# Kernel optimization log

Hardware: AMD Instinct MI355X
Metric: run time of the kernel (lower is better)

Reference implementation:

```python
import jax, jax.numpy as jnp
import numpy as np

OUT_FEATURES = 11008
IN_FEATURES = 4096
GROUP_SIZE = 32
NUM_GROUPS = OUT_FEATURES * IN_FEATURES // GROUP_SIZE        # 1,409,024
NUM_PACKED = NUM_GROUPS * (GROUP_SIZE // 8 * 3)              # 16,908,288 bytes


def block_dequantize_3bit(weight_q3, weight_norm):
    """Unpack 3-bit codes (8 values per 3 bytes) and dequantize to fp32."""
    p = weight_q3.reshape(-1, 3).astype(jnp.int32)  # [N/8, 3] bytes
    b0, b1, b2 = p[:, 0], p[:, 1], p[:, 2]
    q = jnp.stack([
        b0 & 7,
        (b0 >> 3) & 7,
        ((b0 >> 6) & 3) | ((b1 & 1) << 2),
        (b1 >> 1) & 7,
        (b1 >> 4) & 7,
        ((b1 >> 7) & 1) | ((b2 & 3) << 1),
        (b2 >> 2) & 7,
        (b2 >> 5) & 7,
    ], axis=-1)                                     # [N/8, 8] codes in 0..7
    q = q.reshape(NUM_GROUPS, GROUP_SIZE).astype(jnp.float32)
    norm = weight_norm.astype(jnp.float32)[:, None]  # [num_groups, 1]
    w = (q / 7.0) * 2.0 * norm - norm                # map [0,7] -> [-norm, norm]
    return w.reshape(OUT_FEATURES, IN_FEATURES)


def setup_inputs() -> dict:
    key = jax.random.key(0)
    k1, k2, k3, k4 = jax.random.split(key, 4)
    x = jax.random.normal(k1, (4, 128, IN_FEATURES), dtype=jnp.float32)
    weight_q3 = jax.random.randint(k2, (NUM_PACKED,), 0, 256, dtype=jnp.int32)
    weight_norm = (jax.random.uniform(k3, (NUM_GROUPS,), dtype=jnp.float32) * 0.1 + 0.01).astype(jnp.float16)
    bias = jax.random.normal(k4, (OUT_FEATURES,), dtype=jnp.float32) * 0.02
    return {"x": x, "weight_q3": weight_q3, "weight_norm": weight_norm, "bias": bias}


def reference(x, weight_q3, weight_norm, bias):
    w = block_dequantize_3bit(weight_q3, weight_norm)  # [out, in] fp32
    return jnp.einsum('bsd,od->bso', x, w) + bias
```

## Files before the change

### kernel.cpp

```cpp
#include <hip/hip_runtime.h>
#include <hip/hip_fp16.h>

#define M_TOTAL 512
#define N_TOTAL 11008
#define K_TOTAL 4096
#define BM 256
#define BN 32
#define BK 64
#define NT (K_TOTAL / BK)
#define NUM_GROUPS (N_TOTAL * K_TOTAL / 32)
#define LDK 72

typedef short bf16x8 __attribute__((ext_vector_type(8)));
typedef _Float16 f16x8 __attribute__((ext_vector_type(8)));
typedef _Float16 f16x2 __attribute__((ext_vector_type(2)));
typedef float f32x4 __attribute__((ext_vector_type(4)));

__device__ __forceinline__ unsigned int pack2_bf16(float f0, float f1) {
    unsigned int u0 = __builtin_bit_cast(unsigned int, f0) + 0x8000u;
    unsigned int u1 = __builtin_bit_cast(unsigned int, f1) + 0x8000u;
    return (u0 >> 16) | (u1 & 0xFFFF0000u);
}

__device__ __forceinline__ void async_ld16(void* lds, const void* g) {
    __builtin_amdgcn_global_load_lds(
        (const __attribute__((address_space(1))) unsigned int*)g,
        (__attribute__((address_space(3))) unsigned int*)lds, 16, 0, 0);
}

__device__ __forceinline__ int detect_mode_wave(const void* __restrict__ wn) {
    const int lane = threadIdx.x & 63;
    const unsigned short* u16 = (const unsigned short*)wn;
    const float* f32p = (const float*)wn;
    const float vb = __builtin_bit_cast(float, (unsigned int)u16[lane] << 16);
    const float vh = __half2float(__builtin_bit_cast(__half, u16[lane]));
    const float vf = f32p[lane];
    const unsigned long long mb = __ballot(vb > 0.005f && vb < 0.12f);
    const unsigned long long mh = __ballot(vh > 0.005f && vh < 0.12f);
    (void)vf;
    return (mb == ~0ull) ? 2 : ((mh == ~0ull) ? 1 : 0);
}

__global__ void __launch_bounds__(256)
convert_x_kernel(const float* __restrict__ x, unsigned short* __restrict__ xh) {
    const int i = (blockIdx.x * 256 + threadIdx.x) * 4;
    const float4 v = *(const float4*)&x[i];
    const unsigned int p0 = __builtin_bit_cast(unsigned int, __builtin_amdgcn_cvt_pkrtz(v.x, v.y));
    const unsigned int p1 = __builtin_bit_cast(unsigned int, __builtin_amdgcn_cvt_pkrtz(v.z, v.w));
    *(uint2*)&xh[i] = make_uint2(p0, p1);
}

__global__ void __launch_bounds__(512)
norm_pack_kernel(const void* __restrict__ wn, unsigned int* __restrict__ np) {
    const int mode = detect_mode_wave(wn);
    const int g = blockIdx.x * 512 + threadIdx.x;
    if (g >= NUM_GROUPS) return;
    float n;
    if (mode == 0)      n = ((const float*)wn)[g];
    else if (mode == 1) n = __half2float(((const __half*)wn)[g]);
    else                n = __builtin_bit_cast(float,
                            (unsigned int)((const unsigned short*)wn)[g] << 16);
    np[g] = __builtin_bit_cast(unsigned int,
                __builtin_amdgcn_cvt_pkrtz(n * (2.0f / 7.0f), -n));
}

__global__ void __launch_bounds__(512, 4)
l3b_gemm_pipe(const _Float16* __restrict__ xh, const int* __restrict__ wq,
              const unsigned int* __restrict__ np, const float* __restrict__ bias,
              float* __restrict__ out)
{
    __shared__ _Float16 As[2][BM * 64];
    __shared__ _Float16 Bs[2][BN * 64];

    const int tid  = threadIdx.x;

    const int bid   = blockIdx.x;
    const int local = bid >> 3;
    const int m0    = (local & 1) * BM;
    const int n0    = ((local >> 1) + (bid & 7) * 43) * BN;

    const int wid  = tid >> 6;
    const int lane = tid & 63;
    const int quad = lane >> 4;
    const int lm   = lane & 15;
    const int wm   = wid * 32;

    const int bt   = tid;
    const int bn_l = bt >> 3;
    const int bc   = bt & 7;
    const int bkg  = bc >> 2;
    const int bsub = bc & 3;
    const int ldsB = (bn_l << 6) + ((bc ^ (bn_l & 7)) << 3);

    const int au    = tid - 256;
    const int arow0 = au >> 3;
    const int acol  = ((au & 7) ^ ((au >> 3) & 7)) * 8;
    const int aphys = (au & 7) * 8;

    auto stageA = [&](int it, int buf) {
#pragma unroll
        for (int j = 0; j < 8; ++j) {
            const int row = arow0 + j * 32;
            async_ld16((void*)&As[buf][(row << 6) + aphys],
                       &xh[(size_t)(m0 + row) * K_TOTAL + it * 64 + acol]);
        }
    };

    auto loadB = [&](int it, int& b0, int& b1, int& b2, unsigned int& npk) {
        const int g    = (n0 + bn_l) * (K_TOTAL / 32) + it * 2 + bkg;
        const int base = g * 12 + bsub * 3;
        b0 = wq[base]; b1 = wq[base + 1]; b2 = wq[base + 2];
        npk = np[g];
    };

    const __half2 h1024 = __builtin_bit_cast(__half2, 0x64006400u);
    auto decodeB = [&](int b0, int b1, int b2, unsigned int npk, int buf) {
        const __half2 ss = __builtin_bit_cast(__half2,
            __builtin_amdgcn_perm(npk, npk, 0x01000100u));
        const __half2 cc = __builtin_bit_cast(__half2,
            __builtin_amdgcn_perm(npk, npk, 0x03020302u));
        const unsigned int bits =
            (unsigned)b0 | ((unsigned)b1 << 8) | ((unsigned)b2 << 16);
        unsigned int packs[4];
#pragma unroll
        for (int j = 0; j < 4; ++j) {
            const unsigned int q0 = (bits >> (6 * j)) & 7;
            const unsigned int q1 = (bits >> (6 * j + 3)) & 7;
            const __half2 h = __builtin_bit_cast(__half2,
                (q0 | (q1 << 16)) | 0x64006400u);
            const __half2 q = __hsub2(h, h1024);
            packs[j] = __builtin_bit_cast(unsigned int, __hfma2(q, ss, cc));
        }
        *(uint4*)&Bs[buf][ldsB] = make_uint4(packs[0], packs[1], packs[2], packs[3]);
    };

    f32x4 acc[2][2];
#pragma unroll
    for (int i = 0; i < 2; ++i)
#pragma unroll
        for (int j = 0; j < 2; ++j) acc[i][j] = (f32x4){0.f, 0.f, 0.f, 0.f};

    auto mfmaTile = [&](const _Float16* Asb, const _Float16* Bsb) {
#pragma unroll
        for (int ks = 0; ks < 2; ++ks) {
            const int cswz = (((ks * 4 + quad) ^ (lm & 7)) << 3);
            f16x8 aF[2], bF[2];
#pragma unroll
            for (int mi = 0; mi < 2; ++mi)
                aF[mi] = *(const f16x8*)&Asb[((wm + mi * 16 + lm) << 6) + cswz];
#pragma unroll
            for (int ni = 0; ni < 2; ++ni)
                bF[ni] = *(const f16x8*)&Bsb[((ni * 16 + lm) << 6) + cswz];
#pragma unroll
            for (int mi = 0; mi < 2; ++mi)
#pragma unroll
                for (int ni = 0; ni < 2; ++ni)
                    acc[mi][ni] = __builtin_amdgcn_mfma_f32_16x16x32_f16(
                        aF[mi], bF[ni], acc[mi][ni], 0, 0, 0);
        }
    };

    int ba0, ba1, ba2; unsigned int npa;
    int bb0, bb1, bb2; unsigned int npb;

    if (tid < 256) {
        loadB(0, ba0, ba1, ba2, npa);
        decodeB(ba0, ba1, ba2, npa, 0);
        loadB(1, bb0, bb1, bb2, npb);
    } else {
        stageA(0, 0);
    }
    __syncthreads();

    for (int it = 0; it < NT; it += 2) {
        if (tid < 256) {
            if (it + 2 < NT) loadB(it + 2, ba0, ba1, ba2, npa);
            if (it + 1 < NT) decodeB(bb0, bb1, bb2, npb, 1);
        } else {
            if (it + 1 < NT) stageA(it + 1, 1);
        }
        mfmaTile(As[0], Bs[0]);
        __syncthreads();

        if (tid < 256) {
            if (it + 3 < NT) loadB(it + 3, bb0, bb1, bb2, npb);
            if (it + 2 < NT) decodeB(ba0, ba1, ba2, npa, 0);
        } else {
            if (it + 2 < NT) stageA(it + 2, 0);
        }
        mfmaTile(As[1], Bs[1]);
        __syncthreads();
    }

#pragma unroll
    for (int ni = 0; ni < 2; ++ni) {
        const int o  = n0 + ni * 16 + lm;
        const float bv = bias[o];
#pragma unroll
        for (int mi = 0; mi < 2; ++mi) {
#pragma unroll
            for (int r = 0; r < 4; ++r) {
                const int m = m0 + wm + mi * 16 + quad * 4 + r;
                out[m * N_TOTAL + o] = acc[mi][ni][r] + bv;
            }
        }
    }
}

__global__ void __launch_bounds__(256)
l3b_gemm_kernel(const float* __restrict__ x, const int* __restrict__ wq,
                const void* __restrict__ wnorm, const float* __restrict__ bias,
                float* __restrict__ out)
{
    __shared__ unsigned short As[128 * LDK];
    __shared__ unsigned short Bs[64 * LDK];

    const int mode = detect_mode_wave(wnorm);
    const int tid  = threadIdx.x;
    const int m0   = blockIdx.y * 128;
    const int n0   = blockIdx.x * 64;
    const int wid  = tid >> 6;
    const int lane = tid & 63;
    const int quad = lane >> 4;
    const int lm   = lane & 15;
    const int wm   = (wid >> 1) * 64;
    const int wn   = (wid & 1) * 32;

    f32x4 acc[4][2];
#pragma unroll
    for (int i = 0; i < 4; ++i)
#pragma unroll
        for (int j = 0; j < 2; ++j) acc[i][j] = (f32x4){0.f, 0.f, 0.f, 0.f};

    const int ar = tid >> 4;
    const int ac = (tid & 15) * 4;
    const int gin      = tid >> 1;
    const int half     = tid & 1;
    const int bn_local = gin >> 1;
    const int bkg      = gin & 1;

    for (int it = 0; it < NT; ++it) {
        const int k0 = it * BK;
        __syncthreads();
#pragma unroll
        for (int p = 0; p < 8; ++p) {
            const int row = p * 16 + ar;
            const float4 v = *(const float4*)&x[(m0 + row) * K_TOTAL + k0 + ac];
            *(uint2*)&As[row * LDK + ac] =
                make_uint2(pack2_bf16(v.x, v.y), pack2_bf16(v.z, v.w));
        }
        {
            const int g    = (n0 + bn_local) * (K_TOTAL / 32) + it * 2 + bkg;
            const int base = g * 12 + half * 6;
            const int2 w0 = *(const int2*)&wq[base];
            const int2 w1 = *(const int2*)&wq[base + 2];
            const int2 w2 = *(const int2*)&wq[base + 4];
            float nrm;
            if (mode == 0)      nrm = ((const float*)wnorm)[g];
            else if (mode == 1) nrm = __half2float(((const __half*)wnorm)[g]);
            else                nrm = __builtin_bit_cast(float,
                                    (unsigned int)((const unsigned short*)wnorm)[g] << 16);
            const float a = nrm * (2.0f / 7.0f);
            const float b = -nrm;
            const unsigned int bits0 =
                (unsigned)w0.x | ((unsigned)w0.y << 8) | ((unsigned)w1.x << 16);
            const unsigned int bits1 =
                (unsigned)w1.y | ((unsigned)w2.x << 8) | ((unsigned)w2.y << 16);
            unsigned int packs[8];
#pragma unroll
            for (int t3 = 0; t3 < 2; ++t3) {
                const unsigned int bits = t3 ? bits1 : bits0;
#pragma unroll
                for (int j = 0; j < 4; ++j) {
                    const float f0 = fmaf((float)((bits >> (6 * j)) & 7), a, b);
                    const float f1 = fmaf((float)((bits >> (6 * j + 3)) & 7), a, b);
                    packs[t3 * 4 + j] = pack2_bf16(f0, f1);
                }
            }
            unsigned int* dst = (unsigned int*)&Bs[bn_local * LDK + bkg * 32 + half * 16];
            *(uint4*)dst       = make_uint4(packs[0], packs[1], packs[2], packs[3]);
            *(uint4*)(dst + 4) = make_uint4(packs[4], packs[5], packs[6], packs[7]);
        }
        __syncthreads();
#pragma unroll
        for (int ks = 0; ks < 2; ++ks) {
            const int kb = ks * 32 + quad * 8;
            bf16x8 aF[4], bF[2];
#pragma unroll
            for (int mi = 0; mi < 4; ++mi)
                aF[mi] = *(const bf16x8*)&As[(wm + mi * 16 + lm) * LDK + kb];
#pragma unroll
            for (int ni = 0; ni < 2; ++ni)
                bF[ni] = *(const bf16x8*)&Bs[(wn + ni * 16 + lm) * LDK + kb];
#pragma unroll
            for (int mi = 0; mi < 4; ++mi)
#pragma unroll
                for (int ni = 0; ni < 2; ++ni)
                    acc[mi][ni] = __builtin_amdgcn_mfma_f32_16x16x32_bf16(
                        aF[mi], bF[ni], acc[mi][ni], 0, 0, 0);
        }
    }
#pragma unroll
    for (int ni = 0; ni < 2; ++ni) {
        const int o  = n0 + wn + ni * 16 + lm;
        const float bv = bias[o];
#pragma unroll
        for (int mi = 0; mi < 4; ++mi)
#pragma unroll
            for (int r = 0; r < 4; ++r) {
                const int m = m0 + wm + mi * 16 + quad * 4 + r;
                out[m * N_TOTAL + o] = acc[mi][ni][r] + bv;
            }
    }
}

extern "C" void kernel_launch(void* const* d_in, const int* in_sizes, int n_in,
                              void* d_out, int out_size, void* d_ws, size_t ws_size,
                              hipStream_t stream) {
    const float* x    = (const float*)d_in[0];
    const int*   wq   = (const int*)d_in[1];
    const void*  wn   = d_in[2];
    const float* bias = (const float*)d_in[3];
    float* out = (float*)d_out;

    const size_t xh_off = 256;
    const size_t xh_sz  = (size_t)M_TOTAL * K_TOTAL * 2;
    const size_t np_off = xh_off + xh_sz;
    const size_t np_sz  = (size_t)NUM_GROUPS * 4;
    const size_t need   = np_off + np_sz;

    if (ws_size >= need) {
        unsigned short* xh = (unsigned short*)((char*)d_ws + xh_off);
        unsigned int*   np = (unsigned int*)((char*)d_ws + np_off);
        convert_x_kernel<<<(M_TOTAL * K_TOTAL / 4) / 256, 256, 0, stream>>>(x, xh);
        norm_pack_kernel<<<(NUM_GROUPS + 511) / 512, 512, 0, stream>>>(wn, np);
        l3b_gemm_pipe<<<(M_TOTAL / BM) * (N_TOTAL / BN), 512, 0, stream>>>(
            (const _Float16*)xh, wq, np, bias, out);
    } else {
        dim3 grid(N_TOTAL / 64, M_TOTAL / 128);
        l3b_gemm_kernel<<<grid, 256, 0, stream>>>(x, wq, wn, bias, out);
    }
}
```

Baseline: 239.6 us.

## Retile GEMM to 128x64 blocks with unified producers and deeper weight prefetch

Changes the block tile from 256x32 to 128x64, arranges the 8 waves as a 4x2 grid over M and N, and remaps block indices with a new swizzle over 4 M-tiles. Warp specialization is removed: every thread now stages A asynchronously and also loads and decodes B, instead of splitting the work between two halves of the block. Weight prefetch is deepened to three iterations with four rotating register sets, and the occupancy hint is raised from 4 to 6 blocks. The aim is better balance between the A and B loads and more latency hiding. The cost is more register pressure, and each block now reads x tiles for twice as many N columns.

```diff
diff --git a/kernel.cpp b/kernel.cpp
--- a/kernel.cpp
+++ b/kernel.cpp
@@ -4,8 +4,8 @@
 #define M_TOTAL 512
 #define N_TOTAL 11008
 #define K_TOTAL 4096
-#define BM 256
-#define BN 32
+#define BM 128
+#define BN 64
 #define BK 64
 #define NT (K_TOTAL / BK)
 #define NUM_GROUPS (N_TOTAL * K_TOTAL / 32)
@@ -13,7 +13,6 @@
 
 typedef short bf16x8 __attribute__((ext_vector_type(8)));
 typedef _Float16 f16x8 __attribute__((ext_vector_type(8)));
-typedef _Float16 f16x2 __attribute__((ext_vector_type(2)));
 typedef float f32x4 __attribute__((ext_vector_type(4)));
 
 __device__ __forceinline__ unsigned int pack2_bf16(float f0, float f1) {
@@ -64,7 +63,7 @@
                 __builtin_amdgcn_cvt_pkrtz(n * (2.0f / 7.0f), -n));
 }
 
-__global__ void __launch_bounds__(512, 4)
+__global__ void __launch_bounds__(512, 6)
 l3b_gemm_pipe(const _Float16* __restrict__ xh, const int* __restrict__ wq,
               const unsigned int* __restrict__ np, const float* __restrict__ bias,
               float* __restrict__ out)
@@ -74,41 +73,40 @@
 
     const int tid  = threadIdx.x;
 
-    const int bid   = blockIdx.x;
-    const int local = bid >> 3;
-    const int m0    = (local & 1) * BM;
-    const int n0    = ((local >> 1) + (bid & 7) * 43) * BN;
+    const int bid = blockIdx.x;
+    const int w   = (bid & 7) * 86 + (bid >> 3);
+    const int m0  = (w & 3) * BM;
+    const int n0  = (w >> 2) * BN;
 
     const int wid  = tid >> 6;
     const int lane = tid & 63;
     const int quad = lane >> 4;
     const int lm   = lane & 15;
-    const int wm   = wid * 32;
-
-    const int bt   = tid;
-    const int bn_l = bt >> 3;
-    const int bc   = bt & 7;
-    const int bkg  = bc >> 2;
-    const int bsub = bc & 3;
-    const int ldsB = (bn_l << 6) + ((bc ^ (bn_l & 7)) << 3);
-
-    const int au    = tid - 256;
-    const int arow0 = au >> 3;
-    const int acol  = ((au & 7) ^ ((au >> 3) & 7)) * 8;
-    const int aphys = (au & 7) * 8;
+    const int wm   = (wid >> 1) * 32;
+    const int wn_  = (wid & 1) * 32;
+
+    const int arow0 = wid * 8 + (lane >> 3);
+    const int acol  = ((lane & 7) ^ ((lane >> 3) & 7)) * 8;
+    const int aphys = (lane & 7) * 8;
+
+    const int gl   = tid >> 2;
+    const int sub  = tid & 3;
+    const int bn_l = gl >> 1;
+    const int kg   = gl & 1;
+    const int ldsB = (bn_l << 6) + (((kg * 4 + sub) ^ (bn_l & 7)) << 3);
 
     auto stageA = [&](int it, int buf) {
 #pragma unroll
-        for (int j = 0; j < 8; ++j) {
-            const int row = arow0 + j * 32;
+        for (int j = 0; j < 2; ++j) {
+            const int row = arow0 + j * 64;
             async_ld16((void*)&As[buf][(row << 6) + aphys],
                        &xh[(size_t)(m0 + row) * K_TOTAL + it * 64 + acol]);
         }
     };
 
     auto loadB = [&](int it, int& b0, int& b1, int& b2, unsigned int& npk) {
-        const int g    = (n0 + bn_l) * (K_TOTAL / 32) + it * 2 + bkg;
-        const int base = g * 12 + bsub * 3;
+        const int g    = (n0 + bn_l) * (K_TOTAL / 32) + it * 2 + kg;
+        const int base = g * 12 + sub * 3;
         b0 = wq[base]; b1 = wq[base + 1]; b2 = wq[base + 2];
         npk = np[g];
     };
@@ -150,7 +148,7 @@
                 aF[mi] = *(const f16x8*)&Asb[((wm + mi * 16 + lm) << 6) + cswz];
 #pragma unroll
             for (int ni = 0; ni < 2; ++ni)
-                bF[ni] = *(const f16x8*)&Bsb[((ni * 16 + lm) << 6) + cswz];
+                bF[ni] = *(const f16x8*)&Bsb[((wn_ + ni * 16 + lm) << 6) + cswz];
 #pragma unroll
             for (int mi = 0; mi < 2; ++mi)
 #pragma unroll
@@ -160,41 +158,56 @@
         }
     };
 
-    int ba0, ba1, ba2; unsigned int npa;
-    int bb0, bb1, bb2; unsigned int npb;
-
-    if (tid < 256) {
-        loadB(0, ba0, ba1, ba2, npa);
-        decodeB(ba0, ba1, ba2, npa, 0);
-        loadB(1, bb0, bb1, bb2, npb);
-    } else {
-        stageA(0, 0);
-    }
+    int a0, a1, a2; unsigned int an;
+    int b0, b1, b2; unsigned int bn;
+    int c0, c1, c2; unsigned int cn;
+    int d0, d1, d2; unsigned int dn;
+
+    loadB(0, a0, a1, a2, an);
+    loadB(1, b0, b1, b2, bn);
+    loadB(2, c0, c1, c2, cn);
+    stageA(0, 0);
+    decodeB(a0, a1, a2, an, 0);
     __syncthreads();
 
-    for (int it = 0; it < NT; it += 2) {
-        if (tid < 256) {
-            if (it + 2 < NT) loadB(it + 2, ba0, ba1, ba2, npa);
-            if (it + 1 < NT) decodeB(bb0, bb1, bb2, npb, 1);
-        } else {
-            if (it + 1 < NT) stageA(it + 1, 1);
-        }
-        mfmaTile(As[0], Bs[0]);
-        __syncthreads();
-
-        if (tid < 256) {
-            if (it + 3 < NT) loadB(it + 3, bb0, bb1, bb2, npb);
-            if (it + 2 < NT) decodeB(ba0, ba1, ba2, npa, 0);
-        } else {
-            if (it + 2 < NT) stageA(it + 2, 0);
-        }
-        mfmaTile(As[1], Bs[1]);
-        __syncthreads();
+    for (int it = 0; it < NT; it += 4) {
+        {
+            const int t = it;
+            if (t + 1 < NT) stageA(t + 1, 1);
+            if (t + 3 < NT) loadB(t + 3, d0, d1, d2, dn);
+            if (t + 1 < NT) decodeB(b0, b1, b2, bn, 1);
+            mfmaTile(As[0], Bs[0]);
+            __syncthreads();
+        }
+        {
+            const int t = it + 1;
+            if (t + 1 < NT) stageA(t + 1, 0);
+            if (t + 3 < NT) loadB(t + 3, a0, a1, a2, an);
+            if (t + 1 < NT) decodeB(c0, c1, c2, cn, 0);
+            mfmaTile(As[1], Bs[1]);
+            __syncthreads();
+        }
+        {
+            const int t = it + 2;
+            if (t + 1 < NT) stageA(t + 1, 1);
+            if (t + 3 < NT) loadB(t + 3, b0, b1, b2, bn);
+            if (t + 1 < NT) decodeB(d0, d1, d2, dn, 1);
+            mfmaTile(As[0], Bs[0]);
+            __syncthreads();
+        }
+        {
+            const int t = it + 3;
+            if (t + 1 < NT) stageA(t + 1, 0);
+            if (t + 3 < NT) loadB(t + 3, c0, c1, c2, cn);
+            if (t + 1 < NT) decodeB(a0, a1, a2, an, 0);
+            mfmaTile(As[1], Bs[1]);
+            __syncthreads();
+        }
     }
 
 #pragma unroll
     for (int ni = 0; ni < 2; ++ni) {
-        const int o  = n0 + ni * 16 + lm;
+        const int o  = n0 + wn_ + ni * 16 + lm;
         const float bv = bias[o];
 #pragma unroll
         for (int mi = 0; mi < 2; ++mi) {
```

Result: faster. 202.2 us (-15.6%).
